# Performance work log

Hardware: AMD Instinct MI355X
Metric: run time of the kernel (lower is better)

## Reference

```python
import jax, jax.numpy as jnp
import numpy as np

B, N, IN_DIM, OUT_DIM, C = 8, 8192, 1024, 512, 64
TEMPERATURE = 1.0
LN_EPS = 1e-5


def setup_inputs() -> dict:
    key = jax.random.key(0)
    ks = jax.random.split(key, 6)
    node_embeddings = jax.random.normal(ks[0], (B, N, IN_DIM), dtype=jnp.float32)
    node_mask = jnp.zeros((B, N), dtype=bool)  # True => node is masked out
    # xavier_uniform for cluster_centers [C, OUT_DIM]
    lim_c = float(np.sqrt(6.0 / (C + OUT_DIM)))
    cluster_centers = jax.random.uniform(ks[1], (C, OUT_DIM), jnp.float32, -lim_c, lim_c)
    # nn.Linear default init (kaiming-uniform-ish bounds)
    lim_n = float(1.0 / np.sqrt(IN_DIM))
    W_node = jax.random.uniform(ks[2], (IN_DIM, OUT_DIM), jnp.float32, -lim_n, lim_n)
    b_node = jax.random.uniform(ks[3], (OUT_DIM,), jnp.float32, -lim_n, lim_n)
    lim_k = float(1.0 / np.sqrt(OUT_DIM))
    W_cluster = jax.random.uniform(ks[4], (OUT_DIM, OUT_DIM), jnp.float32, -lim_k, lim_k)
    b_cluster = jax.random.uniform(ks[5], (OUT_DIM,), jnp.float32, -lim_k, lim_k)
    ln_gamma = jnp.ones((OUT_DIM,), jnp.float32)
    ln_beta = jnp.zeros((OUT_DIM,), jnp.float32)
    return {
        "node_embeddings": node_embeddings,
        "node_mask": node_mask,
        "cluster_centers": cluster_centers,
        "W_node": W_node,
        "b_node": b_node,
        "W_cluster": W_cluster,
        "b_cluster": b_cluster,
        "ln_gamma": ln_gamma,
        "ln_beta": ln_beta,
    }


def reference(node_embeddings, node_mask, cluster_centers, W_node, b_node,
              W_cluster, b_cluster, ln_gamma, ln_beta):
    # node projection: [B, N, D]
    node_proj = jnp.einsum('bni,io->bno', node_embeddings, W_node) + b_node
    # projected cluster centers (batch-independent): [C, D]
    ccp = cluster_centers @ W_cluster + b_cluster
    # similarities: [B, C, N]
    sims = jnp.einsum('cd,bnd->bcn', ccp, node_proj) / TEMPERATURE
    sims = jnp.where(node_mask[:, None, :], -jnp.inf, sims)
    assignment_weights = jax.nn.softmax(sims, axis=-1)  # dropout is identity in eval
    # aggregate: [B, C, D], residual add of projected centers
    compressed = jnp.einsum('bcn,bnd->bcd', assignment_weights, node_proj) + ccp
    # LayerNorm over last dim
    mu = jnp.mean(compressed, axis=-1, keepdims=True)
    var = jnp.var(compressed, axis=-1, keepdims=True)
    compressed = (compressed - mu) * jax.lax.rsqrt(var + LN_EPS) * ln_gamma + ln_beta
    return compressed, assignment_weights
```

## Files before the change

### kernel.cpp

```cpp
#include <hip/hip_runtime.h>
#include <hip/hip_bf16.h>
#include <math.h>

#define Bn 8
#define Nn 8192
#define KIN 1024
#define DOUT 512
#define NC 64
#define LN_EPS 1e-5f

typedef short bf16x8 __attribute__((ext_vector_type(8)));
typedef short s8v __attribute__((ext_vector_type(8)));
typedef short s4v __attribute__((ext_vector_type(4)));
typedef float f32x4 __attribute__((ext_vector_type(4)));

__device__ __forceinline__ short f2bf(float f) {
    __hip_bfloat16 h = __float2bfloat16(f);
    return __builtin_bit_cast(short, h);
}

__device__ __forceinline__ void load_lds16(const void* g, void* l) {
    __builtin_amdgcn_global_load_lds(
        (const __attribute__((address_space(1))) unsigned int*)g,
        (__attribute__((address_space(3))) unsigned int*)l, 16, 0, 0);
}

__global__ __launch_bounds__(256) void k_prep_w(const float* __restrict__ W,
                                                short* __restrict__ Wt) {
    __shared__ short L[64 * 72];
    const int tid = threadIdx.x;
    const int kt = blockIdx.x >> 3, nt = blockIdx.x & 7;
    const int k0 = kt * 64, n0 = nt * 64;
    {
        int r = tid >> 2, c0 = (tid & 3) * 16;
        const float* g = W + (size_t)(k0 + r) * DOUT + n0 + c0;
        float4 a0 = *reinterpret_cast<const float4*>(g);
        float4 a1 = *reinterpret_cast<const float4*>(g + 4);
        float4 a2 = *reinterpret_cast<const float4*>(g + 8);
        float4 a3 = *reinterpret_cast<const float4*>(g + 12);
        s8v p0, p1;
        p0[0]=f2bf(a0.x); p0[1]=f2bf(a0.y); p0[2]=f2bf(a0.z); p0[3]=f2bf(a0.w);
        p0[4]=f2bf(a1.x); p0[5]=f2bf(a1.y); p0[6]=f2bf(a1.z); p0[7]=f2bf(a1.w);
        p1[0]=f2bf(a2.x); p1[1]=f2bf(a2.y); p1[2]=f2bf(a2.z); p1[3]=f2bf(a2.w);
        p1[4]=f2bf(a3.x); p1[5]=f2bf(a3.y); p1[6]=f2bf(a3.z); p1[7]=f2bf(a3.w);
        *reinterpret_cast<s8v*>(&L[r * 72 + c0]) = p0;
        *reinterpret_cast<s8v*>(&L[r * 72 + c0 + 8]) = p1;
    }
    __syncthreads();
    {
        int n = tid >> 2, kc = (tid & 3) * 16;
        s8v y0, y1;
#pragma unroll
        for (int j = 0; j < 8; ++j) y0[j] = L[(kc + j) * 72 + n];
#pragma unroll
        for (int j = 0; j < 8; ++j) y1[j] = L[(kc + 8 + j) * 72 + n];
        short* o = Wt + (size_t)(n0 + n) * KIN + k0 + kc;
        *reinterpret_cast<s8v*>(o) = y0;
        *reinterpret_cast<s8v*>(o + 8) = y1;
    }
}

__global__ __launch_bounds__(256) void k_prep_c(
    const float* __restrict__ cc, const float* __restrict__ Wc,
    const float* __restrict__ bc, float* __restrict__ ccp_f,
    short* __restrict__ ccp_bf) {
    __shared__ float ccs[512];
    const int tid = threadIdx.x, c = blockIdx.x;
    ccs[tid] = cc[c * DOUT + tid];
    ccs[tid + 256] = cc[c * DOUT + tid + 256];
    __syncthreads();
    float a0 = bc[tid], a1 = bc[tid + 256];
    for (int k = 0; k < DOUT; ++k) {
        float s = ccs[k];
        a0 += s * Wc[(size_t)k * DOUT + tid];
        a1 += s * Wc[(size_t)k * DOUT + tid + 256];
    }
    ccp_f[c * DOUT + tid] = a0;
    ccp_f[c * DOUT + tid + 256] = a1;
    ccp_bf[c * DOUT + tid] = f2bf(a0);
    ccp_bf[c * DOUT + tid + 256] = f2bf(a1);
}

__global__ __launch_bounds__(256, 2) void k_gemm1(
    const float* __restrict__ A, const short* __restrict__ Wt,
    const float* __restrict__ bias, short* __restrict__ proj,
    short* __restrict__ projT) {
    __shared__ short smem[2 * 64 * 40 + 2 * 512 * 32];
    short (*As)[64 * 40] = reinterpret_cast<short(*)[64 * 40]>(smem);
    short (*Bs)[512 * 32] = reinterpret_cast<short(*)[512 * 32]>(smem + 2 * 64 * 40);
    const int tid = threadIdx.x, lane = tid & 63, wv = tid >> 6;
    const int quad = lane >> 4, l15 = lane & 15;
    const int m0 = blockIdx.x * 64;

    f32x4 acc[4][8];
#pragma unroll
    for (int i = 0; i < 4; ++i)
#pragma unroll
        for (int j = 0; j < 8; ++j) acc[i][j] = (f32x4){0.f, 0.f, 0.f, 0.f};

    const int ar = tid >> 2;
    const int ac2 = (tid & 3) * 8;
    const float* Ag = A + (size_t)(m0 + ar) * KIN + ac2;

    {
#pragma unroll
        for (int i = 0; i < 8; ++i) {
            int c = i * 256 + tid;
            int n = c >> 2, kc = c & 3;
            load_lds16(Wt + (size_t)n * KIN + kc * 8,
                       &Bs[0][(i * 256 + wv * 64) * 8]);
        }
        float4 a0 = *reinterpret_cast<const float4*>(Ag);
        float4 a1 = *reinterpret_cast<const float4*>(Ag + 4);
        s8v p;
        p[0]=f2bf(a0.x); p[1]=f2bf(a0.y); p[2]=f2bf(a0.z); p[3]=f2bf(a0.w);
        p[4]=f2bf(a1.x); p[5]=f2bf(a1.y); p[6]=f2bf(a1.z); p[7]=f2bf(a1.w);
        *reinterpret_cast<s8v*>(&As[0][ar * 40 + ac2]) = p;
    }
    __syncthreads();

    int cur = 0;
    for (int it = 0; it < KIN / 32; ++it) {
        const bool pf = (it + 1 < KIN / 32);
        float4 a0, a1;
        if (pf) {
            const int k1 = (it + 1) * 32;
            a0 = *reinterpret_cast<const float4*>(Ag + k1);
            a1 = *reinterpret_cast<const float4*>(Ag + k1 + 4);
#pragma unroll
            for (int i = 0; i < 8; ++i) {
                int c = i * 256 + tid;
                int n = c >> 2, kc = c & 3;
                load_lds16(Wt + (size_t)n * KIN + k1 + kc * 8,
                           &Bs[cur ^ 1][(i * 256 + wv * 64) * 8]);
            }
        }
        bf16x8 af[4], bfr[8];
#pragma unroll
        for (int mi = 0; mi < 4; ++mi)
            af[mi] = *reinterpret_cast<const bf16x8*>(&As[cur][(mi * 16 + l15) * 40 + quad * 8]);
#pragma unroll
        for (int ni = 0; ni < 8; ++ni)
            bfr[ni] = *reinterpret_cast<const bf16x8*>(&Bs[cur][(wv * 128 + ni * 16 + l15) * 32 + quad * 8]);
#pragma unroll
        for (int mi = 0; mi < 4; ++mi)
#pragma unroll
            for (int ni = 0; ni < 8; ++ni)
                acc[mi][ni] = __builtin_amdgcn_mfma_f32_16x16x32_bf16(af[mi], bfr[ni], acc[mi][ni], 0, 0, 0);
        if (pf) {
            s8v p;
            p[0]=f2bf(a0.x); p[1]=f2bf(a0.y); p[2]=f2bf(a0.z); p[3]=f2bf(a0.w);
            p[4]=f2bf(a1.x); p[5]=f2bf(a1.y); p[6]=f2bf(a1.z); p[7]=f2bf(a1.w);
            *reinterpret_cast<s8v*>(&As[cur ^ 1][ar * 40 + ac2]) = p;
        }
        __syncthreads();
        cur ^= 1;
    }

    short* T = smem;
#pragma unroll
    for (int ni = 0; ni < 8; ++ni) {
        int col = wv * 128 + ni * 16 + l15;
        float bv = bias[col];
#pragma unroll
        for (int mi = 0; mi < 4; ++mi) {
            int ml = mi * 16 + quad * 4;
            s4v t;
#pragma unroll
            for (int r = 0; r < 4; ++r) {
                short v = f2bf(acc[mi][ni][r] + bv);
                t[r] = v;
                proj[(size_t)(m0 + ml + r) * DOUT + col] = v;
            }
            *reinterpret_cast<s4v*>(&T[col * 72 + ml]) = t;
        }
    }
    __syncthreads();
#pragma unroll
    for (int p = 0; p < 16; ++p) {
        int col = p * 32 + (tid >> 3);
        int ch = (tid & 7) * 8;
        s8v v = *reinterpret_cast<const s8v*>(&T[col * 72 + ch]);
        *reinterpret_cast<s8v*>(projT + (size_t)col * (Bn * Nn) + m0 + ch) = v;
    }
}

__global__ __launch_bounds__(256) void k_sims(
    const short* __restrict__ ccp_bf, const short* __restrict__ proj,
    float* __restrict__ sims) {
    __shared__ short As[2][64 * 32];
    __shared__ short Bs[2][128 * 32];
    const int tid = threadIdx.x, lane = tid & 63, wv = tid >> 6;
    const int quad = lane >> 4, l15 = lane & 15;
    const int b = blockIdx.x >> 6, nt = blockIdx.x & 63;
    const int n0 = nt * 128;
    const int wm = wv & 1, wn = wv >> 1;

    f32x4 acc[2][4];
#pragma unroll
    for (int i = 0; i < 2; ++i)
#pragma unroll
        for (int j = 0; j < 4; ++j) acc[i][j] = (f32x4){0.f, 0.f, 0.f, 0.f};

    auto stage = [&](int buf, int k0) {
        {
            int r = tid >> 2, kc = tid & 3;
            load_lds16(ccp_bf + (size_t)r * DOUT + k0 + kc * 8,
                       &As[buf][(wv * 64) * 8]);
        }
#pragma unroll
        for (int i = 0; i < 2; ++i) {
            int c = i * 256 + tid;
            int r = c >> 2, kc = c & 3;
            load_lds16(proj + (size_t)(b * Nn + n0 + r) * DOUT + k0 + kc * 8,
                       &Bs[buf][(i * 256 + wv * 64) * 8]);
        }
    };

    stage(0, 0);
    __syncthreads();
    int cur = 0;
    for (int it = 0; it < DOUT / 32; ++it) {
        if (it + 1 < DOUT / 32) stage(cur ^ 1, (it + 1) * 32);
        bf16x8 af[2], bfr[4];
#pragma unroll
        for (int mi = 0; mi < 2; ++mi)
            af[mi] = *reinterpret_cast<const bf16x8*>(&As[cur][(wm * 32 + mi * 16 + l15) * 32 + quad * 8]);
#pragma unroll
        for (int ni = 0; ni < 4; ++ni)
            bfr[ni] = *reinterpret_cast<const bf16x8*>(&Bs[cur][(wn * 64 + ni * 16 + l15) * 32 + quad * 8]);
#pragma unroll
        for (int mi = 0; mi < 2; ++mi)
#pragma unroll
            for (int ni = 0; ni < 4; ++ni)
                acc[mi][ni] = __builtin_amdgcn_mfma_f32_16x16x32_bf16(af[mi], bfr[ni], acc[mi][ni], 0, 0, 0);
        __syncthreads();
        cur ^= 1;
    }
#pragma unroll
    for (int mi = 0; mi < 2; ++mi)
#pragma unroll
        for (int ni = 0; ni < 4; ++ni)
#pragma unroll
            for (int r = 0; r < 4; ++r) {
                int c = wm * 32 + mi * 16 + quad * 4 + r;
                int n = n0 + wn * 64 + ni * 16 + l15;
                sims[((size_t)b * NC + c) * Nn + n] = acc[mi][ni][r];
            }
}

__global__ __launch_bounds__(256) void k_softmax(
    float* __restrict__ aw, const unsigned char* __restrict__ mask,
    short* __restrict__ aw_bf) {
    __shared__ float red[8];
    const int tid = threadIdx.x, lane = tid & 63, wv = tid >> 6;
    const int b = blockIdx.x >> 6, c = blockIdx.x & 63;
    float* p = aw + ((size_t)b * NC + c) * Nn;
    short* q = aw_bf + ((size_t)b * NC + c) * Nn;
    const unsigned char* mp = mask + b * Nn;

    float v[32];
    float mx = -INFINITY;
#pragma unroll
    for (int i = 0; i < 32; ++i) {
        int idx = tid + i * 256;
        float x = p[idx];
        if (mp[idx]) x = -INFINITY;
        v[i] = x;
        mx = fmaxf(mx, x);
    }
    for (int off = 32; off; off >>= 1) mx = fmaxf(mx, __shfl_xor(mx, off));
    if (lane == 0) red[wv] = mx;
    __syncthreads();
    mx = fmaxf(fmaxf(red[0], red[1]), fmaxf(red[2], red[3]));
    __syncthreads();

    float s = 0.f;
#pragma unroll
    for (int i = 0; i < 32; ++i) {
        v[i] = expf(v[i] - mx);
        s += v[i];
    }
    for (int off = 32; off; off >>= 1) s += __shfl_xor(s, off);
    if (lane == 0) red[wv] = s;
    __syncthreads();
    s = red[0] + red[1] + red[2] + red[3];
    float inv = 1.f / s;
#pragma unroll
    for (int i = 0; i < 32; ++i) {
        int idx = tid + i * 256;
        float w = v[i] * inv;
        p[idx] = w;
        q[idx] = f2bf(w);
    }
}

__global__ __launch_bounds__(256) void k_agg(
    const short* __restrict__ aw_bf, const short* __restrict__ projT,
    float* __restrict__ partial) {
    __shared__ short As[2][64 * 32];
    __shared__ short Bs[2][128 * 32];
    const int tid = threadIdx.x, lane = tid & 63, wv = tid >> 6;
    const int quad = lane >> 4, l15 = lane & 15;
    const int b = blockIdx.x >> 5, dt = (blockIdx.x >> 3) & 3, ksp = blockIdx.x & 7;
    const int d0 = dt * 128;
    const int wm = wv & 1, wn = wv >> 1;

    f32x4 acc[2][4];
#pragma unroll
    for (int i = 0; i < 2; ++i)
#pragma unroll
        for (int j = 0; j < 4; ++j) acc[i][j] = (f32x4){0.f, 0.f, 0.f, 0.f};

    auto stage = [&](int buf, int nb) {
        {
            int r = tid >> 2, kc = tid & 3;
            load_lds16(aw_bf + ((size_t)b * NC + r) * Nn + nb + kc * 8,
                       &As[buf][(wv * 64) * 8]);
        }
#pragma unroll
        for (int i = 0; i < 2; ++i) {
            int c = i * 256 + tid;
            int r = c >> 2, kc = c & 3;
            load_lds16(projT + (size_t)(d0 + r) * (Bn * Nn) + b * Nn + nb + kc * 8,
                       &Bs[buf][(i * 256 + wv * 64) * 8]);
        }
    };

    stage(0, ksp * 1024);
    __syncthreads();
    int cur = 0;
    for (int it = 0; it < 32; ++it) {
        if (it + 1 < 32) stage(cur ^ 1, ksp * 1024 + (it + 1) * 32);
        bf16x8 af[2], bfr[4];
#pragma unroll
        for (int mi = 0; mi < 2; ++mi)
            af[mi] = *reinterpret_cast<const bf16x8*>(&As[cur][(wm * 32 + mi * 16 + l15) * 32 + quad * 8]);
#pragma unroll
        for (int ni = 0; ni < 4; ++ni)
            bfr[ni] = *reinterpret_cast<const bf16x8*>(&Bs[cur][(wn * 64 + ni * 16 + l15) * 32 + quad * 8]);
#pragma unroll
        for (int mi = 0; mi < 2; ++mi)
#pragma unroll
            for (int ni = 0; ni < 4; ++ni)
                acc[mi][ni] = __builtin_amdgcn_mfma_f32_16x16x32_bf16(af[mi], bfr[ni], acc[mi][ni], 0, 0, 0);
        __syncthreads();
        cur ^= 1;
    }
#pragma unroll
    for (int mi = 0; mi < 2; ++mi)
#pragma unroll
        for (int ni = 0; ni < 4; ++ni)
#pragma unroll
            for (int r = 0; r < 4; ++r) {
                int c = wm * 32 + mi * 16 + quad * 4 + r;
                int d = d0 + wn * 64 + ni * 16 + l15;
                partial[(((size_t)b * 8 + ksp) * NC + c) * DOUT + d] = acc[mi][ni][r];
            }
}

__global__ __launch_bounds__(256) void k_ln(
    const float* __restrict__ partial, const float* __restrict__ ccp,
    const float* __restrict__ gamma, const float* __restrict__ beta,
    float* __restrict__ out) {
    __shared__ float red[16];
    const int tid = threadIdx.x, lane = tid & 63, wv = tid >> 6;
    const int b = blockIdx.x >> 6, c = blockIdx.x & 63;
    float v0 = ccp[c * DOUT + tid], v1 = ccp[c * DOUT + tid + 256];
#pragma unroll
    for (int ks = 0; ks < 8; ++ks) {
        const float* pp = partial + (((size_t)b * 8 + ks) * NC + c) * DOUT;
        v0 += pp[tid];
        v1 += pp[tid + 256];
    }
    float s = v0 + v1, sq = v0 * v0 + v1 * v1;
    for (int off = 32; off; off >>= 1) {
        s += __shfl_xor(s, off);
        sq += __shfl_xor(sq, off);
    }
    if (lane == 0) { red[wv] = s; red[8 + wv] = sq; }
    __syncthreads();
    s = red[0] + red[1] + red[2] + red[3];
    sq = red[8] + red[9] + red[10] + red[11];
    float mu = s * (1.f / 512.f);
    float var = sq * (1.f / 512.f) - mu * mu;
    float rs = rsqrtf(var + LN_EPS);
    size_t base = ((size_t)b * NC + c) * DOUT;
    out[base + tid] = (v0 - mu) * rs * gamma[tid] + beta[tid];
    out[base + tid + 256] = (v1 - mu) * rs * gamma[tid + 256] + beta[tid + 256];
}

extern "C" void kernel_launch(void* const* d_in, const int* in_sizes, int n_in,
                              void* d_out, int out_size, void* d_ws, size_t ws_size,
                              hipStream_t stream) {
    const float* node_emb = (const float*)d_in[0];
    const unsigned char* mask = (const unsigned char*)d_in[1];
    const float* cc = (const float*)d_in[2];
    const float* Wn = (const float*)d_in[3];
    const float* bn = (const float*)d_in[4];
    const float* Wc = (const float*)d_in[5];
    const float* bc = (const float*)d_in[6];
    const float* gamma = (const float*)d_in[7];
    const float* beta = (const float*)d_in[8];
    float* out = (float*)d_out;

    char* ws = (char*)d_ws;
    short* proj   = (short*)(ws);
    short* projT  = (short*)(ws + 67108864);
    short* aw_bf  = (short*)(ws + 134217728);
    float* ccp_f  = (float*)(ws + 142606336);
    short* ccp_bf = (short*)(ws + 142737408);
    short* Wt     = (short*)(ws + 142802944);
    float* partial= (float*)(ws + 143851520);

    float* sims = out + (size_t)Bn * NC * DOUT;

    k_prep_w<<<128, 256, 0, stream>>>(Wn, Wt);
    k_prep_c<<<64, 256, 0, stream>>>(cc, Wc, bc, ccp_f, ccp_bf);
    k_gemm1<<<1024, 256, 0, stream>>>(node_emb, Wt, bn, proj, projT);
    k_sims<<<512, 256, 0, stream>>>(ccp_bf, proj, sims);
    k_softmax<<<512, 256, 0, stream>>>(sims, mask, aw_bf);
    k_agg<<<256, 256, 0, stream>>>(aw_bf, projT, partial);
    k_ln<<<512, 256, 0, stream>>>(partial, ccp_f, gamma, beta, out);
}
```

Measured before the change: 551.8 us.

## Enlarge gemm1 tile to 128 rows with 512 threads and XOR-swizzle LDS

The node-projection GEMM now uses 128-row tiles and 8 waves per block in a 2x4 wave grid, so each staged 512-column weight tile is reused across twice as many rows and the weight traffic per output drops. The epilogue writes the transposed tile in two halves to fit the shared buffer. An XOR swizzle on the 16-byte k-chunk position is applied to the LDS staging and fragment reads in gemm1, sims and agg kernels to reduce LDS bank conflicts. The cost is more LDS per block and more registers per block, which may lower occupancy, plus extra barriers in the epilogue.

```diff
diff --git a/kernel.cpp b/kernel.cpp
--- a/kernel.cpp
+++ b/kernel.cpp
@@ -81,16 +81,18 @@
     ccp_bf[c * DOUT + tid + 256] = f2bf(a1);
 }
 
-__global__ __launch_bounds__(256, 2) void k_gemm1(
+__global__ __launch_bounds__(512, 2) void k_gemm1(
     const float* __restrict__ A, const short* __restrict__ Wt,
     const float* __restrict__ bias, short* __restrict__ proj,
     short* __restrict__ projT) {
-    __shared__ short smem[2 * 64 * 40 + 2 * 512 * 32];
-    short (*As)[64 * 40] = reinterpret_cast<short(*)[64 * 40]>(smem);
-    short (*Bs)[512 * 32] = reinterpret_cast<short(*)[512 * 32]>(smem + 2 * 64 * 40);
+    __shared__ short smem[2 * 128 * 40 + 2 * 512 * 32];
+    short (*As)[128 * 40] = reinterpret_cast<short(*)[128 * 40]>(smem);
+    short (*Bs)[512 * 32] = reinterpret_cast<short(*)[512 * 32]>(smem + 2 * 128 * 40);
     const int tid = threadIdx.x, lane = tid & 63, wv = tid >> 6;
     const int quad = lane >> 4, l15 = lane & 15;
-    const int m0 = blockIdx.x * 64;
+    const int wm = wv & 1, wn = wv >> 1;
+    const int m0 = blockIdx.x * 128;
+    const int qs = quad ^ ((l15 >> 1) & 3);
 
     f32x4 acc[4][8];
 #pragma unroll
@@ -104,11 +106,12 @@
 
     {
 #pragma unroll
-        for (int i = 0; i < 8; ++i) {
-            int c = i * 256 + tid;
+        for (int i = 0; i < 4; ++i) {
+            int c = i * 512 + tid;
             int n = c >> 2, kc = c & 3;
-            load_lds16(Wt + (size_t)n * KIN + kc * 8,
-                       &Bs[0][(i * 256 + wv * 64) * 8]);
+            int kq = kc ^ ((n >> 1) & 3);
+            load_lds16(Wt + (size_t)n * KIN + kq * 8,
+                       &Bs[0][(i * 512 + wv * 64) * 8]);
         }
         float4 a0 = *reinterpret_cast<const float4*>(Ag);
         float4 a1 = *reinterpret_cast<const float4*>(Ag + 4);
@@ -128,20 +131,21 @@
             a0 = *reinterpret_cast<const float4*>(Ag + k1);
             a1 = *reinterpret_cast<const float4*>(Ag + k1 + 4);
 #pragma unroll
-            for (int i = 0; i < 8; ++i) {
-                int c = i * 256 + tid;
+            for (int i = 0; i < 4; ++i) {
+                int c = i * 512 + tid;
                 int n = c >> 2, kc = c & 3;
-                load_lds16(Wt + (size_t)n * KIN + k1 + kc * 8,
-                           &Bs[cur ^ 1][(i * 256 + wv * 64) * 8]);
+                int kq = kc ^ ((n >> 1) & 3);
+                load_lds16(Wt + (size_t)n * KIN + k1 + kq * 8,
+                           &Bs[cur ^ 1][(i * 512 + wv * 64) * 8]);
             }
         }
         bf16x8 af[4], bfr[8];
 #pragma unroll
         for (int mi = 0; mi < 4; ++mi)
-            af[mi] = *reinterpret_cast<const bf16x8*>(&As[cur][(mi * 16 + l15) * 40 + quad * 8]);
+            af[mi] = *reinterpret_cast<const bf16x8*>(&As[cur][(wm * 64 + mi * 16 + l15) * 40 + quad * 8]);
 #pragma unroll
         for (int ni = 0; ni < 8; ++ni)
-            bfr[ni] = *reinterpret_cast<const bf16x8*>(&Bs[cur][(wv * 128 + ni * 16 + l15) * 32 + quad * 8]);
+            bfr[ni] = *reinterpret_cast<const bf16x8*>(&Bs[cur][(wn * 128 + ni * 16 + l15) * 32 + qs * 8]);
 #pragma unroll
         for (int mi = 0; mi < 4; ++mi)
 #pragma unroll
@@ -158,30 +162,39 @@
     }
 
     short* T = smem;
-#pragma unroll
-    for (int ni = 0; ni < 8; ++ni) {
-        int col = wv * 128 + ni * 16 + l15;
-        float bv = bias[col];
-#pragma unroll
-        for (int mi = 0; mi < 4; ++mi) {
-            int ml = mi * 16 + quad * 4;
-            s4v t;
-#pragma unroll
-            for (int r = 0; r < 4; ++r) {
-                short v = f2bf(acc[mi][ni][r] + bv);
-                t[r] = v;
-                proj[(size_t)(m0 + ml + r) * DOUT + col] = v;
+    float bv[8];
+#pragma unroll
+    for (int ni = 0; ni < 8; ++ni) bv[ni] = bias[wn * 128 + ni * 16 + l15];
+
+#pragma unroll
+    for (int h = 0; h < 2; ++h) {
+        if (wm == h) {
+#pragma unroll
+            for (int ni = 0; ni < 8; ++ni) {
+                int col = wn * 128 + ni * 16 + l15;
+#pragma unroll
+                for (int mi = 0; mi < 4; ++mi) {
+                    int ml = mi * 16 + quad * 4;
+                    s4v t;
+#pragma unroll
+                    for (int r = 0; r < 4; ++r) {
+                        short v = f2bf(acc[mi][ni][r] + bv[ni]);
+                        t[r] = v;
+                        proj[(size_t)(m0 + h * 64 + ml + r) * DOUT + col] = v;
+                    }
+                    *reinterpret_cast<s4v*>(&T[col * 72 + ml]) = t;
+                }
             }
-            *reinterpret_cast<s4v*>(&T[col * 72 + ml]) = t;
-        }
-    }
-    __syncthreads();
-#pragma unroll
-    for (int p = 0; p < 16; ++p) {
-        int col = p * 32 + (tid >> 3);
-        int ch = (tid & 7) * 8;
-        s8v v = *reinterpret_cast<const s8v*>(&T[col * 72 + ch]);
-        *reinterpret_cast<s8v*>(projT + (size_t)col * (Bn * Nn) + m0 + ch) = v;
+        }
+        __syncthreads();
+#pragma unroll
+        for (int p = 0; p < 8; ++p) {
+            int col = p * 64 + (tid >> 3);
+            int ch = (tid & 7) * 8;
+            s8v v = *reinterpret_cast<const s8v*>(&T[col * 72 + ch]);
+            *reinterpret_cast<s8v*>(projT + (size_t)col * (Bn * Nn) + m0 + h * 64 + ch) = v;
+        }
+        __syncthreads();
     }
 }
 
@@ -195,6 +208,7 @@
     const int b = blockIdx.x >> 6, nt = blockIdx.x & 63;
     const int n0 = nt * 128;
     const int wm = wv & 1, wn = wv >> 1;
+    const int qs = quad ^ ((l15 >> 1) & 3);
 
     f32x4 acc[2][4];
 #pragma unroll
@@ -205,14 +219,16 @@
     auto stage = [&](int buf, int k0) {
         {
             int r = tid >> 2, kc = tid & 3;
-            load_lds16(ccp_bf + (size_t)r * DOUT + k0 + kc * 8,
+            int kq = kc ^ ((r >> 1) & 3);
+            load_lds16(ccp_bf + (size_t)r * DOUT + k0 + kq * 8,
                        &As[buf][(wv * 64) * 8]);
         }
 #pragma unroll
         for (int i = 0; i < 2; ++i) {
             int c = i * 256 + tid;
             int r = c >> 2, kc = c & 3;
-            load_lds16(proj + (size_t)(b * Nn + n0 + r) * DOUT + k0 + kc * 8,
+            int kq = kc ^ ((r >> 1) & 3);
+            load_lds16(proj + (size_t)(b * Nn + n0 + r) * DOUT + k0 + kq * 8,
                        &Bs[buf][(i * 256 + wv * 64) * 8]);
         }
     };
@@ -225,10 +241,10 @@
         bf16x8 af[2], bfr[4];
 #pragma unroll
         for (int mi = 0; mi < 2; ++mi)
-            af[mi] = *reinterpret_cast<const bf16x8*>(&As[cur][(wm * 32 + mi * 16 + l15) * 32 + quad * 8]);
+            af[mi] = *reinterpret_cast<const bf16x8*>(&As[cur][(wm * 32 + mi * 16 + l15) * 32 + qs * 8]);
 #pragma unroll
         for (int ni = 0; ni < 4; ++ni)
-            bfr[ni] = *reinterpret_cast<const bf16x8*>(&Bs[cur][(wn * 64 + ni * 16 + l15) * 32 + quad * 8]);
+            bfr[ni] = *reinterpret_cast<const bf16x8*>(&Bs[cur][(wn * 64 + ni * 16 + l15) * 32 + qs * 8]);
 #pragma unroll
         for (int mi = 0; mi < 2; ++mi)
 #pragma unroll
@@ -305,6 +321,7 @@
     const int b = blockIdx.x >> 5, dt = (blockIdx.x >> 3) & 3, ksp = blockIdx.x & 7;
     const int d0 = dt * 128;
     const int wm = wv & 1, wn = wv >> 1;
+    const int qs = quad ^ ((l15 >> 1) & 3);
 
     f32x4 acc[2][4];
 #pragma unroll
@@ -315,14 +332,16 @@
     auto stage = [&](int buf, int nb) {
         {
             int r = tid >> 2, kc = tid & 3;
-            load_lds16(aw_bf + ((size_t)b * NC + r) * Nn + nb + kc * 8,
+            int kq = kc ^ ((r >> 1) & 3);
+            load_lds16(aw_bf + ((size_t)b * NC + r) * Nn + nb + kq * 8,
                        &As[buf][(wv * 64) * 8]);
         }
 #pragma unroll
         for (int i = 0; i < 2; ++i) {
             int c = i * 256 + tid;
             int r = c >> 2, kc = c & 3;
-            load_lds16(projT + (size_t)(d0 + r) * (Bn * Nn) + b * Nn + nb + kc * 8,
+            int kq = kc ^ ((r >> 1) & 3);
+            load_lds16(projT + (size_t)(d0 + r) * (Bn * Nn) + b * Nn + nb + kq * 8,
                        &Bs[buf][(i * 256 + wv * 64) * 8]);
         }
     };
@@ -335,10 +354,10 @@
         bf16x8 af[2], bfr[4];
 #pragma unroll
         for (int mi = 0; mi < 2; ++mi)
-            af[mi] = *reinterpret_cast<const bf16x8*>(&As[cur][(wm * 32 + mi * 16 + l15) * 32 + quad * 8]);
+            af[mi] = *reinterpret_cast<const bf16x8*>(&As[cur][(wm * 32 + mi * 16 + l15) * 32 + qs * 8]);
 #pragma unroll
         for (int ni = 0; ni < 4; ++ni)
-            bfr[ni] = *reinterpret_cast<const bf16x8*>(&Bs[cur][(wn * 64 + ni * 16 + l15) * 32 + quad * 8]);
+            bfr[ni] = *reinterpret_cast<const bf16x8*>(&Bs[cur][(wn * 64 + ni * 16 + l15) * 32 + qs * 8]);
 #pragma unroll
         for (int mi = 0; mi < 2; ++mi)
 #pragma unroll
@@ -417,7 +436,7 @@
 
     k_prep_w<<<128, 256, 0, stream>>>(Wn, Wt);
     k_prep_c<<<64, 256, 0, stream>>>(cc, Wc, bc, ccp_f, ccp_bf);
-    k_gemm1<<<1024, 256, 0, stream>>>(node_emb, Wt, bn, proj, projT);
+    k_gemm1<<<512, 512, 0, stream>>>(node_emb, Wt, bn, proj, projT);
     k_sims<<<512, 256, 0, stream>>>(ccp_bf, proj, sims);
     k_softmax<<<512, 256, 0, stream>>>(sims, mask, aw_bf);
     k_agg<<<256, 256, 0, stream>>>(aw_bf, projT, partial);
```

Measured after the change: 530.8 us. 3.8% less time.
